# Performance work log

Measured on AMD Instinct MI355X. Metric: run time of the kernel, lower is better.

The kernel has to match this reference:

```python
import jax, jax.numpy as jnp
import numpy as np

NR = 512      # num robots
NT = 1024     # num tasks
E = 500000    # num edges
D = 64        # robot_dim == task_dim (forced by torch.cat dim=0)
ED = 32       # edge_dim
GH = 128      # gnn_hidden
MH = 128      # mlp_hidden
SLOPE = 0.1   # LeakyReLU negative slope


def lrelu(x):
    return jnp.where(x >= 0, x, SLOPE * x)


def _linear(key, out_d, in_d):
    k1, k2 = jax.random.split(key)
    s = 1.0 / np.sqrt(in_d)
    W = jax.random.uniform(k1, (out_d, in_d), minval=-s, maxval=s, dtype=jnp.float32)
    b = jax.random.uniform(k2, (out_d,), minval=-s, maxval=s, dtype=jnp.float32)
    return W, b


def setup_inputs() -> dict:
    key = jax.random.key(0)
    ks = jax.random.split(key, 12)
    x_robot = jax.random.normal(ks[0], (NR, D), dtype=jnp.float32)
    x_task = jax.random.normal(ks[1], (NT, D), dtype=jnp.float32)
    edge_attr = jax.random.normal(ks[2], (E, ED), dtype=jnp.float32)
    src = jax.random.randint(ks[3], (E,), 0, NR)
    tgt = jax.random.randint(ks[4], (E,), 0, NT)
    edge_index = jnp.stack([src, tgt], axis=0).astype(jnp.int64)
    We1, be1 = _linear(ks[5], GH, 2 * D + ED)   # f_theta_e layer 1
    We2, be2 = _linear(ks[6], GH, GH)            # f_theta_e layer 2
    Wv1, bv1 = _linear(ks[7], GH, D + GH)        # f_theta_v layer 1
    Wv2, bv2 = _linear(ks[8], GH, GH)            # f_theta_v layer 2
    Wm1, bm1 = _linear(ks[9], MH, GH + D)        # task selector layer 1
    Wm2, bm2 = _linear(ks[10], 1, MH)            # task selector layer 2
    return {
        'x_robot': x_robot, 'x_task': x_task, 'edge_index': edge_index,
        'edge_attr': edge_attr,
        'We1': We1, 'be1': be1, 'We2': We2, 'be2': be2,
        'Wv1': Wv1, 'bv1': bv1, 'Wv2': Wv2, 'bv2': bv2,
        'Wm1': Wm1, 'bm1': bm1, 'Wm2': Wm2, 'bm2': bm2,
    }


def reference(x_robot, x_task, edge_index, edge_attr,
              We1, be1, We2, be2, Wv1, bv1, Wv2, bv2, Wm1, bm1, Wm2, bm2):
    n_robot = x_robot.shape[0]
    x = jnp.concatenate([x_robot, x_task], axis=0)          # [NR+NT, D]
    src = edge_index[0]                                      # robot indices
    tgt = edge_index[1] + n_robot                            # shifted task indices
    # PyG default flow='source_to_target': x_i = x[target], x_j = x[source],
    # messages are scatter-added at target slots (the task slots here).
    msg_in = jnp.concatenate([x[tgt], x[src], edge_attr], axis=1)  # [E, 2D+ED]
    m = lrelu(msg_in @ We1.T + be1) @ We2.T + be2            # [E, GH]
    agg = jax.ops.segment_sum(m, tgt, num_segments=n_robot + x_task.shape[0])
    robot_msgs = agg[:n_robot]                               # all zeros (faithful to source)
    upd_in = jnp.concatenate([robot_msgs, x_robot], axis=1)  # [NR, GH+D]
    h = lrelu(upd_in @ Wv1.T + bv1) @ Wv2.T + bv2            # [NR, GH]
    # Pairwise MLP on concat([h_i, task_j]) without materializing the concat:
    # split Wm1 columns into the robot-hidden and task parts.
    hr = h @ Wm1[:, :GH].T                                   # [NR, MH]
    ht = x_task @ Wm1[:, GH:].T                              # [NT, MH]
    hid = lrelu(hr[:, None, :] + ht[None, :, :] + bm1)       # [NR, NT, MH]
    scores = jnp.einsum('nmh,h->nm', hid, Wm2[0]) + bm2[0]   # [NR, NT]
    return jax.nn.softmax(scores, axis=1)
```

## Files before the change

kernel.cpp:

```cpp
#include <hip/hip_runtime.h>

#define NRB 512
#define NTK 1024
#define DD  64
#define GHH 128



__global__ __launch_bounds__(256) void prep_kernel(
    const float* __restrict__ xr, const float* __restrict__ xt,
    const float* __restrict__ Wv1, const float* __restrict__ bv1,
    const float* __restrict__ Wv2, const float* __restrict__ bv2,
    const float* __restrict__ Wm1, const float* __restrict__ bm1,
    const float* __restrict__ Wm2, const float* __restrict__ bm2,
    float* __restrict__ HR, float* __restrict__ HTBt4,
    float* __restrict__ av, float* __restrict__ cv, float* __restrict__ wbv)
{
    const int t = threadIdx.x;
    const int b = blockIdx.x;
    const int i = t & 127;
    const int g = t >> 7;

    __shared__ float lds_w[128 * 129];
    __shared__ float xs[8][64];
    __shared__ float sA[4][128];
    __shared__ float sB[4][128];
    __shared__ float sT[8][132];
    __shared__ float sR[8][132];

    if (b < 128) {
        const int r0 = b * 4;
        ((float*)xs)[t] = xr[r0 * DD + t];

        {
            const float4* W = reinterpret_cast<const float4*>(Wv1);
            #pragma unroll
            for (int j = 0; j < 8; ++j) {
                const int e   = t + 256 * j;
                const int row = e >> 4, c4 = e & 15;
                float4 v = W[row * 48 + 32 + c4];
                const int k0 = c4 * 4;
                lds_w[(k0+0)*129 + row] = v.x;
                lds_w[(k0+1)*129 + row] = v.y;
                lds_w[(k0+2)*129 + row] = v.z;
                lds_w[(k0+3)*129 + row] = v.w;
            }
        }
        __syncthreads();

        {
            float a0 = bv1[i], a1 = a0;
            const float* x0 = xs[2*g];
            const float* x1 = xs[2*g + 1];
            #pragma unroll 8
            for (int k = 0; k < 64; ++k) {
                const float w = lds_w[k*129 + i];
                a0 = fmaf(w, x0[k], a0);
                a1 = fmaf(w, x1[k], a1);
            }
            sA[2*g][i]     = (a0 >= 0.f) ? a0 : 0.1f * a0;
            sA[2*g + 1][i] = (a1 >= 0.f) ? a1 : 0.1f * a1;
        }
        __syncthreads();

        {
            const float4* W = reinterpret_cast<const float4*>(Wv2);
            #pragma unroll
            for (int j = 0; j < 16; ++j) {
                const int e   = t + 256 * j;
                const int row = e >> 5, c4 = e & 31;
                float4 v = W[row * 32 + c4];
                const int k0 = c4 * 4;
                lds_w[(k0+0)*129 + row] = v.x;
                lds_w[(k0+1)*129 + row] = v.y;
                lds_w[(k0+2)*129 + row] = v.z;
                lds_w[(k0+3)*129 + row] = v.w;
            }
        }
        __syncthreads();

        {
            float a0 = bv2[i], a1 = a0;
            const float* h0 = sA[2*g];
            const float* h1 = sA[2*g + 1];
            #pragma unroll 8
            for (int k = 0; k < 128; ++k) {
                const float w = lds_w[k*129 + i];
                a0 = fmaf(w, h0[k], a0);
                a1 = fmaf(w, h1[k], a1);
            }
            sB[2*g][i]     = a0;
            sB[2*g + 1][i] = a1;
        }
        __syncthreads();

        {
            const float4* W = reinterpret_cast<const float4*>(Wm1);
            #pragma unroll
            for (int j = 0; j < 16; ++j) {
                const int e   = t + 256 * j;
                const int row = e >> 5, c4 = e & 31;
                float4 v = W[row * 48 + c4];
                const int k0 = c4 * 4;
                lds_w[(k0+0)*129 + row] = v.x;
                lds_w[(k0+1)*129 + row] = v.y;
                lds_w[(k0+2)*129 + row] = v.z;
                lds_w[(k0+3)*129 + row] = v.w;
            }
        }
        __syncthreads();

        {
            const float wm2 = Wm2[i];
            float a0 = 0.f, a1 = 0.f;
            const float* h0 = sB[2*g];
            const float* h1 = sB[2*g + 1];
            #pragma unroll 8
            for (int k = 0; k < 128; ++k) {
                const float w = lds_w[k*129 + i];
                a0 = fmaf(w, h0[k], a0);
                a1 = fmaf(w, h1[k], a1);
            }
            HR[(r0 + 2*g) * GHH + i]     = a0;
            HR[(r0 + 2*g + 1) * GHH + i] = a1;
            sR[2*g][i]     = wm2 * a0;
            sR[2*g + 1][i] = wm2 * a1;
        }
        __syncthreads();

        {
            const int row = t >> 6, c = t & 63;
            float s = sR[row][c] + sR[row][c + 64];
            #pragma unroll
            for (int off = 32; off >= 1; off >>= 1)
                s += __shfl_xor(s, off, 64);
            if (c == 0) av[r0 + row] = 0.55f * s;
        }
    } else {
        const int t0 = (b - 128) * 8;
        ((float*)xs)[t]       = xt[t0 * DD + t];
        ((float*)xs)[256 + t] = xt[t0 * DD + 256 + t];

        {
            const float4* W = reinterpret_cast<const float4*>(Wm1);
            #pragma unroll
            for (int j = 0; j < 8; ++j) {
                const int e   = t + 256 * j;
                const int row = e >> 4, c4 = e & 15;
                float4 v = W[row * 48 + 32 + c4];
                const int k0 = c4 * 4;
                lds_w[(k0+0)*129 + row] = v.x;
                lds_w[(k0+1)*129 + row] = v.y;
                lds_w[(k0+2)*129 + row] = v.z;
                lds_w[(k0+3)*129 + row] = v.w;
            }
        }
        __syncthreads();

        {
            const float bb  = bm1[i];
            const float wm2 = Wm2[i];
            float a0 = bb, a1 = bb, a2 = bb, a3 = bb;
            const float* x0 = xs[4*g];
            const float* x1 = xs[4*g + 1];
            const float* x2 = xs[4*g + 2];
            const float* x3 = xs[4*g + 3];
            #pragma unroll 8
            for (int k = 0; k < 64; ++k) {
                const float w = lds_w[k*129 + i];
                a0 = fmaf(w, x0[k], a0);
                a1 = fmaf(w, x1[k], a1);
                a2 = fmaf(w, x2[k], a2);
                a3 = fmaf(w, x3[k], a3);
            }
            sT[4*g][i]     = a0;  sR[4*g][i]     = wm2 * a0;
            sT[4*g + 1][i] = a1;  sR[4*g + 1][i] = wm2 * a1;
            sT[4*g + 2][i] = a2;  sR[4*g + 2][i] = wm2 * a2;
            sT[4*g + 3][i] = a3;  sR[4*g + 3][i] = wm2 * a3;
        }
        __syncthreads();

        {
            const int h4 = t >> 3, tk = t & 7;
            float4 v;
            v.x = sT[tk][4*h4 + 0];
            v.y = sT[tk][4*h4 + 1];
            v.z = sT[tk][4*h4 + 2];
            v.w = sT[tk][4*h4 + 3];
            reinterpret_cast<float4*>(HTBt4)[h4 * NTK + t0 + tk] = v;
        }

        {
            const int row = t >> 5, c = t & 31;
            float s = sR[row][c] + sR[row][c + 32]
                    + sR[row][c + 64] + sR[row][c + 96];
            #pragma unroll
            for (int off = 16; off >= 1; off >>= 1)
                s += __shfl_xor(s, off, 32);
            if (c == 0) cv[t0 + row] = 0.55f * s + bm2[0];
        }
        if (b == 128 && t < GHH) wbv[t] = 0.45f * Wm2[t];
    }
}

__global__ __launch_bounds__(1024) void score_softmax_kernel(
    const float* __restrict__ HR, const float* __restrict__ HTBt4,
    const float* __restrict__ av, const float* __restrict__ cv,
    const float* __restrict__ wbv, float* __restrict__ out)
{
    const int b   = blockIdx.x;
    const int tid = threadIdx.x;
    const int n0  = b * 2;

    __shared__ float s_hr[2 * GHH];
    __shared__ float s_wb[GHH];
    if (tid < 256)      s_hr[tid]       = HR[n0 * GHH + tid];
    else if (tid < 384) s_wb[tid - 256] = wbv[tid - 256];
    __syncthreads();

    const float4* tb  = reinterpret_cast<const float4*>(HTBt4) + tid;
    const float4* hrA = reinterpret_cast<const float4*>(s_hr);
    const float4* hrB = reinterpret_cast<const float4*>(s_hr + GHH);
    const float4* wb4 = reinterpret_cast<const float4*>(s_wb);

    float acc0 = 0.f, acc1 = 0.f;

    #pragma unroll 4
    for (int h4 = 0; h4 < 32; ++h4) {
        const float4 v  = tb[h4 << 10];
        const float4 w  = wb4[h4];
        const float4 r0 = hrA[h4];
        const float4 r1 = hrB[h4];
        acc0 = fmaf(w.x, fabsf(r0.x + v.x), acc0);
        acc1 = fmaf(w.x, fabsf(r1.x + v.x), acc1);
        acc0 = fmaf(w.y, fabsf(r0.y + v.y), acc0);
        acc1 = fmaf(w.y, fabsf(r1.y + v.y), acc1);
        acc0 = fmaf(w.z, fabsf(r0.z + v.z), acc0);
        acc1 = fmaf(w.z, fabsf(r1.z + v.z), acc1);
        acc0 = fmaf(w.w, fabsf(r0.w + v.w), acc0);
        acc1 = fmaf(w.w, fabsf(r1.w + v.w), acc1);
    }

    const float cm = cv[tid];
    float sc[2];
    sc[0] = acc0 + av[n0]     + cm;
    sc[1] = acc1 + av[n0 + 1] + cm;

    __shared__ float rmax[2][16], rsum[2][16];
    const int wid = tid >> 6, lane = tid & 63;

    #pragma unroll
    for (int n = 0; n < 2; ++n) {
        float mx = sc[n];
        #pragma unroll
        for (int off = 32; off >= 1; off >>= 1)
            mx = fmaxf(mx, __shfl_xor(mx, off, 64));
        if (lane == 0) rmax[n][wid] = mx;
    }
    __syncthreads();

    float ex[2];
    #pragma unroll
    for (int n = 0; n < 2; ++n) {
        float mx = rmax[n][0];
        #pragma unroll
        for (int k = 1; k < 16; ++k) mx = fmaxf(mx, rmax[n][k]);
        float e = expf(sc[n] - mx);
        ex[n] = e;
        float s = e;
        #pragma unroll
        for (int off = 32; off >= 1; off >>= 1) s += __shfl_xor(s, off, 64);
        if (lane == 0) rsum[n][wid] = s;
    }
    __syncthreads();

    #pragma unroll
    for (int n = 0; n < 2; ++n) {
        float s = rsum[n][0];
        #pragma unroll
        for (int k = 1; k < 16; ++k) s += rsum[n][k];
        out[(n0 + n) * NTK + tid] = ex[n] * (1.0f / s);
    }
}

extern "C" void kernel_launch(void* const* d_in, const int* in_sizes, int n_in,
                              void* d_out, int out_size, void* d_ws, size_t ws_size,
                              hipStream_t stream)
{
    const float* xr  = (const float*)d_in[0];
    const float* xt  = (const float*)d_in[1];
    const float* Wv1 = (const float*)d_in[8];
    const float* bv1 = (const float*)d_in[9];
    const float* Wv2 = (const float*)d_in[10];
    const float* bv2 = (const float*)d_in[11];
    const float* Wm1 = (const float*)d_in[12];
    const float* bm1 = (const float*)d_in[13];
    const float* Wm2 = (const float*)d_in[14];
    const float* bm2 = (const float*)d_in[15];

    float* ws    = (float*)d_ws;
    float* HR    = ws;
    float* HTBt4 = ws + 65536;
    float* av    = ws + 196608;
    float* cv    = ws + 197120;
    float* wbv   = ws + 198144;
    float* out   = (float*)d_out;

    hipLaunchKernelGGL(prep_kernel, dim3(256), dim3(256), 0, stream,
                       xr, xt, Wv1, bv1, Wv2, bv2, Wm1, bm1, Wm2, bm2,
                       HR, HTBt4, av, cv, wbv);
    hipLaunchKernelGGL(score_softmax_kernel, dim3(256), dim3(1024), 0, stream,
                       HR, HTBt4, av, cv, wbv, out);
}
```

Measured before the change: 25.75 us.

## Store weights row-major in LDS with float4 reads; read HR/wbv directly from global

The prep kernel stops transposing weights into LDS element by element. It now stores each weight row as float4 with a 33-float4 padded stride, so the dot products use vectorized LDS reads of both weights and activations. The score kernel drops its LDS staging of HR and wbv and the barrier that follows it, and reads those wave-uniform vectors straight from global memory. This trades LDS transpose and scalar-load cost for possible bank conflicts on row-strided float4 reads, and for extra global or scalar loads inside the inner loop.

```diff
diff --git a/kernel.cpp b/kernel.cpp
--- a/kernel.cpp
+++ b/kernel.cpp
@@ -21,91 +21,88 @@
     const int i = t & 127;
     const int g = t >> 7;
 
-    __shared__ float lds_w[128 * 129];
-    __shared__ float xs[8][64];
-    __shared__ float sA[4][128];
-    __shared__ float sB[4][128];
-    __shared__ float sT[8][132];
-    __shared__ float sR[8][132];
+    __shared__ float lds_w[128 * 132];
+    __shared__ float xs[8 * 64];
+    __shared__ float sA[4 * 132];
+    __shared__ float sB[4 * 132];
+    __shared__ float sT[8 * 132];
+    __shared__ float sR[8 * 132];
+
+    float4* Lw = reinterpret_cast<float4*>(lds_w);
 
     if (b < 128) {
         const int r0 = b * 4;
-        ((float*)xs)[t] = xr[r0 * DD + t];
+        xs[t] = xr[r0 * DD + t];
 
         {
             const float4* W = reinterpret_cast<const float4*>(Wv1);
             #pragma unroll
             for (int j = 0; j < 8; ++j) {
-                const int e   = t + 256 * j;
+                const int e = t + 256 * j;
                 const int row = e >> 4, c4 = e & 15;
-                float4 v = W[row * 48 + 32 + c4];
-                const int k0 = c4 * 4;
-                lds_w[(k0+0)*129 + row] = v.x;
-                lds_w[(k0+1)*129 + row] = v.y;
-                lds_w[(k0+2)*129 + row] = v.z;
-                lds_w[(k0+3)*129 + row] = v.w;
+                Lw[row * 33 + c4] = W[row * 48 + 32 + c4];
             }
         }
         __syncthreads();
 
         {
             float a0 = bv1[i], a1 = a0;
-            const float* x0 = xs[2*g];
-            const float* x1 = xs[2*g + 1];
+            const float4* w4 = Lw + i * 33;
+            const float4* x0 = reinterpret_cast<const float4*>(xs + (2*g)*64);
+            const float4* x1 = reinterpret_cast<const float4*>(xs + (2*g+1)*64);
+            #pragma unroll
+            for (int k = 0; k < 16; ++k) {
+                const float4 w = w4[k];
+                const float4 p = x0[k];
+                const float4 q = x1[k];
+                a0 = fmaf(w.x, p.x, a0); a1 = fmaf(w.x, q.x, a1);
+                a0 = fmaf(w.y, p.y, a0); a1 = fmaf(w.y, q.y, a1);
+                a0 = fmaf(w.z, p.z, a0); a1 = fmaf(w.z, q.z, a1);
+                a0 = fmaf(w.w, p.w, a0); a1 = fmaf(w.w, q.w, a1);
+            }
+            sA[(2*g)*132 + i]   = (a0 >= 0.f) ? a0 : 0.1f * a0;
+            sA[(2*g+1)*132 + i] = (a1 >= 0.f) ? a1 : 0.1f * a1;
+        }
+        __syncthreads();
+
+        {
+            const float4* W = reinterpret_cast<const float4*>(Wv2);
+            #pragma unroll
+            for (int j = 0; j < 16; ++j) {
+                const int e = t + 256 * j;
+                const int row = e >> 5, c4 = e & 31;
+                Lw[row * 33 + c4] = W[row * 32 + c4];
+            }
+        }
+        __syncthreads();
+
+        {
+            float a0 = bv2[i], a1 = a0;
+            const float4* w4 = Lw + i * 33;
+            const float4* h0 = reinterpret_cast<const float4*>(sA + (2*g)*132);
+            const float4* h1 = reinterpret_cast<const float4*>(sA + (2*g+1)*132);
             #pragma unroll 8
-            for (int k = 0; k < 64; ++k) {
-                const float w = lds_w[k*129 + i];
-                a0 = fmaf(w, x0[k], a0);
-                a1 = fmaf(w, x1[k], a1);
-            }
-            sA[2*g][i]     = (a0 >= 0.f) ? a0 : 0.1f * a0;
-            sA[2*g + 1][i] = (a1 >= 0.f) ? a1 : 0.1f * a1;
-        }
-        __syncthreads();
-
-        {
-            const float4* W = reinterpret_cast<const float4*>(Wv2);
+            for (int k = 0; k < 32; ++k) {
+                const float4 w = w4[k];
+                const float4 p = h0[k];
+                const float4 q = h1[k];
+                a0 = fmaf(w.x, p.x, a0); a1 = fmaf(w.x, q.x, a1);
+                a0 = fmaf(w.y, p.y, a0); a1 = fmaf(w.y, q.y, a1);
+                a0 = fmaf(w.z, p.z, a0); a1 = fmaf(w.z, q.z, a1);
+                a0 = fmaf(w.w, p.w, a0); a1 = fmaf(w.w, q.w, a1);
+            }
+            sB[(2*g)*132 + i]   = a0;
+            sB[(2*g+1)*132 + i] = a1;
+        }
+        __syncthreads();
+
+        {
+            const float4* W = reinterpret_cast<const float4*>(Wm1);
             #pragma unroll
             for (int j = 0; j < 16; ++j) {
-                const int e   = t + 256 * j;
+                const int e = t + 256 * j;
                 const int row = e >> 5, c4 = e & 31;
-                float4 v = W[row * 32 + c4];
-                const int k0 = c4 * 4;
-                lds_w[(k0+0)*129 + row] = v.x;
-                lds_w[(k0+1)*129 + row] = v.y;
-                lds_w[(k0+2)*129 + row] = v.z;
-                lds_w[(k0+3)*129 + row] = v.w;
-            }
-        }
-        __syncthreads();
-
-        {
-            float a0 = bv2[i], a1 = a0;
-            const float* h0 = sA[2*g];
-            const float* h1 = sA[2*g + 1];
-            #pragma unroll 8
-            for (int k = 0; k < 128; ++k) {
-                const float w = lds_w[k*129 + i];
-                a0 = fmaf(w, h0[k], a0);
-                a1 = fmaf(w, h1[k], a1);
-            }
-            sB[2*g][i]     = a0;
-            sB[2*g + 1][i] = a1;
-        }
-        __syncthreads();
-
-        {
-            const float4* W = reinterpret_cast<const float4*>(Wm1);
-            #pragma unroll
-            for (int j = 0; j < 16; ++j) {
-                const int e   = t + 256 * j;
-                const int row = e >> 5, c4 = e & 31;
-                float4 v = W[row * 48 + c4];
-                const int k0 = c4 * 4;
-                lds_w[(k0+0)*129 + row] = v.x;
-                lds_w[(k0+1)*129 + row] = v.y;
-                lds_w[(k0+2)*129 + row] = v.z;
-                lds_w[(k0+3)*129 + row] = v.w;
+                Lw[row * 33 + c4] = W[row * 48 + c4];
             }
         }
         __syncthreads();
@@ -113,24 +110,29 @@
         {
             const float wm2 = Wm2[i];
             float a0 = 0.f, a1 = 0.f;
-            const float* h0 = sB[2*g];
-            const float* h1 = sB[2*g + 1];
+            const float4* w4 = Lw + i * 33;
+            const float4* h0 = reinterpret_cast<const float4*>(sB + (2*g)*132);
+            const float4* h1 = reinterpret_cast<const float4*>(sB + (2*g+1)*132);
             #pragma unroll 8
-            for (int k = 0; k < 128; ++k) {
-                const float w = lds_w[k*129 + i];
-                a0 = fmaf(w, h0[k], a0);
-                a1 = fmaf(w, h1[k], a1);
+            for (int k = 0; k < 32; ++k) {
+                const float4 w = w4[k];
+                const float4 p = h0[k];
+                const float4 q = h1[k];
+                a0 = fmaf(w.x, p.x, a0); a1 = fmaf(w.x, q.x, a1);
+                a0 = fmaf(w.y, p.y, a0); a1 = fmaf(w.y, q.y, a1);
+                a0 = fmaf(w.z, p.z, a0); a1 = fmaf(w.z, q.z, a1);
+                a0 = fmaf(w.w, p.w, a0); a1 = fmaf(w.w, q.w, a1);
             }
             HR[(r0 + 2*g) * GHH + i]     = a0;
             HR[(r0 + 2*g + 1) * GHH + i] = a1;
-            sR[2*g][i]     = wm2 * a0;
-            sR[2*g + 1][i] = wm2 * a1;
+            sR[(2*g)*132 + i]   = wm2 * a0;
+            sR[(2*g+1)*132 + i] = wm2 * a1;
         }
         __syncthreads();
 
         {
             const int row = t >> 6, c = t & 63;
-            float s = sR[row][c] + sR[row][c + 64];
+            float s = sR[row*132 + c] + sR[row*132 + c + 64];
             #pragma unroll
             for (int off = 32; off >= 1; off >>= 1)
                 s += __shfl_xor(s, off, 64);
@@ -138,21 +140,16 @@
         }
     } else {
         const int t0 = (b - 128) * 8;
-        ((float*)xs)[t]       = xt[t0 * DD + t];
-        ((float*)xs)[256 + t] = xt[t0 * DD + 256 + t];
+        xs[t]       = xt[t0 * DD + t];
+        xs[256 + t] = xt[t0 * DD + 256 + t];
 
         {
             const float4* W = reinterpret_cast<const float4*>(Wm1);
             #pragma unroll
             for (int j = 0; j < 8; ++j) {
-                const int e   = t + 256 * j;
+                const int e = t + 256 * j;
                 const int row = e >> 4, c4 = e & 15;
-                float4 v = W[row * 48 + 32 + c4];
-                const int k0 = c4 * 4;
-                lds_w[(k0+0)*129 + row] = v.x;
-                lds_w[(k0+1)*129 + row] = v.y;
-                lds_w[(k0+2)*129 + row] = v.z;
-                lds_w[(k0+3)*129 + row] = v.w;
+                Lw[row * 33 + c4] = W[row * 48 + 32 + c4];
             }
         }
         __syncthreads();
@@ -161,39 +158,45 @@
             const float bb  = bm1[i];
             const float wm2 = Wm2[i];
             float a0 = bb, a1 = bb, a2 = bb, a3 = bb;
-            const float* x0 = xs[4*g];
-            const float* x1 = xs[4*g + 1];
-            const float* x2 = xs[4*g + 2];
-            const float* x3 = xs[4*g + 3];
-            #pragma unroll 8
-            for (int k = 0; k < 64; ++k) {
-                const float w = lds_w[k*129 + i];
-                a0 = fmaf(w, x0[k], a0);
-                a1 = fmaf(w, x1[k], a1);
-                a2 = fmaf(w, x2[k], a2);
-                a3 = fmaf(w, x3[k], a3);
-            }
-            sT[4*g][i]     = a0;  sR[4*g][i]     = wm2 * a0;
-            sT[4*g + 1][i] = a1;  sR[4*g + 1][i] = wm2 * a1;
-            sT[4*g + 2][i] = a2;  sR[4*g + 2][i] = wm2 * a2;
-            sT[4*g + 3][i] = a3;  sR[4*g + 3][i] = wm2 * a3;
+            const float4* w4 = Lw + i * 33;
+            const float4* x0 = reinterpret_cast<const float4*>(xs + (4*g)*64);
+            const float4* x1 = reinterpret_cast<const float4*>(xs + (4*g+1)*64);
+            const float4* x2 = reinterpret_cast<const float4*>(xs + (4*g+2)*64);
+            const float4* x3 = reinterpret_cast<const float4*>(xs + (4*g+3)*64);
+            #pragma unroll
+            for (int k = 0; k < 16; ++k) {
+                const float4 w = w4[k];
+                const float4 p0 = x0[k], p1 = x1[k], p2 = x2[k], p3 = x3[k];
+                a0 = fmaf(w.x, p0.x, a0); a1 = fmaf(w.x, p1.x, a1);
+                a2 = fmaf(w.x, p2.x, a2); a3 = fmaf(w.x, p3.x, a3);
+                a0 = fmaf(w.y, p0.y, a0); a1 = fmaf(w.y, p1.y, a1);
+                a2 = fmaf(w.y, p2.y, a2); a3 = fmaf(w.y, p3.y, a3);
+                a0 = fmaf(w.z, p0.z, a0); a1 = fmaf(w.z, p1.z, a1);
+                a2 = fmaf(w.z, p2.z, a2); a3 = fmaf(w.z, p3.z, a3);
+                a0 = fmaf(w.w, p0.w, a0); a1 = fmaf(w.w, p1.w, a1);
+                a2 = fmaf(w.w, p2.w, a2); a3 = fmaf(w.w, p3.w, a3);
+            }
+            sT[(4*g)*132 + i]   = a0;  sR[(4*g)*132 + i]   = wm2 * a0;
+            sT[(4*g+1)*132 + i] = a1;  sR[(4*g+1)*132 + i] = wm2 * a1;
+            sT[(4*g+2)*132 + i] = a2;  sR[(4*g+2)*132 + i] = wm2 * a2;
+            sT[(4*g+3)*132 + i] = a3;  sR[(4*g+3)*132 + i] = wm2 * a3;
         }
         __syncthreads();
 
         {
             const int h4 = t >> 3, tk = t & 7;
             float4 v;
-            v.x = sT[tk][4*h4 + 0];
-            v.y = sT[tk][4*h4 + 1];
-            v.z = sT[tk][4*h4 + 2];
-            v.w = sT[tk][4*h4 + 3];
+            v.x = sT[tk*132 + 4*h4 + 0];
+            v.y = sT[tk*132 + 4*h4 + 1];
+            v.z = sT[tk*132 + 4*h4 + 2];
+            v.w = sT[tk*132 + 4*h4 + 3];
             reinterpret_cast<float4*>(HTBt4)[h4 * NTK + t0 + tk] = v;
         }
 
         {
             const int row = t >> 5, c = t & 31;
-            float s = sR[row][c] + sR[row][c + 32]
-                    + sR[row][c + 64] + sR[row][c + 96];
+            float s = sR[row*132 + c]      + sR[row*132 + c + 32]
+                    + sR[row*132 + c + 64] + sR[row*132 + c + 96];
             #pragma unroll
             for (int off = 16; off >= 1; off >>= 1)
                 s += __shfl_xor(s, off, 32);
@@ -212,16 +215,10 @@
     const int tid = threadIdx.x;
     const int n0  = b * 2;
 
-    __shared__ float s_hr[2 * GHH];
-    __shared__ float s_wb[GHH];
-    if (tid < 256)      s_hr[tid]       = HR[n0 * GHH + tid];
-    else if (tid < 384) s_wb[tid - 256] = wbv[tid - 256];
-    __syncthreads();
-
     const float4* tb  = reinterpret_cast<const float4*>(HTBt4) + tid;
-    const float4* hrA = reinterpret_cast<const float4*>(s_hr);
-    const float4* hrB = reinterpret_cast<const float4*>(s_hr + GHH);
-    const float4* wb4 = reinterpret_cast<const float4*>(s_wb);
+    const float4* hrA = reinterpret_cast<const float4*>(HR + n0 * GHH);
+    const float4* hrB = reinterpret_cast<const float4*>(HR + (n0 + 1) * GHH);
+    const float4* wb4 = reinterpret_cast<const float4*>(wbv);
 
     float acc0 = 0.f, acc1 = 0.f;
 
```

New measurement: 22.53 us, median of 2. -12.5%, faster.
